# Kernel optimization log

Measured on AMD Instinct MI355X. Metric: run time of the kernel, lower is better.

The kernel has to match this reference:

```python
import jax, jax.numpy as jnp
import numpy as np

N_NODES, IN_F, HIDDEN, N_EDGES, N_TRAIN, N_CLASS = 50000, 64, 512, 160000, 80000, 7
BN_EPS = 1e-5

def _lin(k, fin, fout):
    return jax.random.normal(k, (fin, fout), jnp.float32) * 0.05, jnp.zeros((fout,), jnp.float32)

def setup_inputs() -> dict:
    key = jax.random.key(0)
    ks = jax.random.split(key, 12)
    x = jax.random.normal(ks[0], (N_NODES, IN_F), jnp.float32)
    edge_index = jax.random.randint(ks[1], (2, N_EDGES), 0, N_NODES, jnp.int32)
    train_edge_id = jax.random.randint(ks[2], (N_TRAIN,), 0, N_EDGES, jnp.int32)
    W1, b1 = _lin(ks[3], IN_F, HIDDEN)
    W2, b2 = _lin(ks[4], HIDDEN, HIDDEN)
    W3, b3 = _lin(ks[5], HIDDEN, HIDDEN)
    W4, b4 = _lin(ks[6], HIDDEN, HIDDEN)
    lin1_W, lin1_b = _lin(ks[7], HIDDEN, HIDDEN)
    lin2_W, lin2_b = _lin(ks[8], HIDDEN, HIDDEN)
    fc2_W, fc2_b = _lin(ks[9], HIDDEN, N_CLASS)
    ones = jnp.ones((HIDDEN,), jnp.float32); zeros = jnp.zeros((HIDDEN,), jnp.float32)
    return dict(x=x, edge_index=edge_index, train_edge_id=train_edge_id,
                W1=W1, b1=b1, W2=W2, b2=b2, W3=W3, b3=b3,
                bn1_g=ones, bn1_b=zeros, bn1_m=zeros, bn1_v=ones, eps1=jnp.float32(0.0),
                W4=W4, b4=b4, bn2_g=ones, bn2_b=zeros, bn2_m=zeros, bn2_v=ones, eps2=jnp.float32(0.0),
                lin1_W=lin1_W, lin1_b=lin1_b, lin2_W=lin2_W, lin2_b=lin2_b,
                fc2_W=fc2_W, fc2_b=fc2_b)

def _gin_agg(h, src, dst, eps):
    # PyG GINConv: (1+eps)*x_i + sum_{j in N(i)} x_j, messages flow src->dst
    agg = jax.ops.segment_sum(h[src], dst, num_segments=N_NODES)
    return (1.0 + eps) * h + agg

def _bn(h, g, b, m, v):
    return (h - m) * jax.lax.rsqrt(v + BN_EPS) * g + b

def reference(x, edge_index, train_edge_id, W1, b1, W2, b2, W3, b3,
              bn1_g, bn1_b, bn1_m, bn1_v, eps1,
              W4, b4, bn2_g, bn2_b, bn2_m, bn2_v, eps2,
              lin1_W, lin1_b, lin2_W, lin2_b, fc2_W, fc2_b):
    src, dst = edge_index[0], edge_index[1]
    h = _gin_agg(x, src, dst, eps1)
    h = jax.nn.relu(h @ W1 + b1)
    h = jax.nn.relu(h @ W2 + b2)
    h = jax.nn.relu(h @ W3 + b3)
    h = _bn(h, bn1_g, bn1_b, bn1_m, bn1_v)
    # gin_convs[0]: agg -> Linear+ReLU -> BN
    h = _gin_agg(h, src, dst, eps2)
    h = jax.nn.relu(h @ W4 + b4)
    h = _bn(h, bn2_g, bn2_b, bn2_m, bn2_v)
    # node MLP head (dropout = identity in eval)
    h = jax.nn.relu(h @ lin1_W + lin1_b)
    h = h @ lin2_W + lin2_b
    # edge-gather fusion (feature_fusion=None -> elementwise mul)
    node_id = edge_index[:, train_edge_id]  # [2, T]
    x1 = h[node_id[0]]
    x2 = h[node_id[1]]
    return (x1 * x2) @ fc2_W + fc2_b  # [T, class_num]
```

## Files before the change

kernel.cpp:

```cpp
#include <hip/hip_runtime.h>

#define N_NODES 50000
#define MPAD    50048
#define IN_F    64
#define HIDDEN  512
#define N_EDGES 160000
#define N_TRAIN 80000
#define N_CLASS 7
#define BN_EPS  1e-5f

#define MT      (MPAD / 128)
#define NT      4
#define FULLGRP ((MT / 8) * 32)

typedef short  bf16x8 __attribute__((ext_vector_type(8)));
typedef float  f32x4  __attribute__((ext_vector_type(4)));
typedef unsigned short ushort_t;

__device__ __forceinline__ ushort_t f2b(float v) {
    union { float f; unsigned int u; } c; c.f = v;
    unsigned int x = c.u;
    unsigned int r = (x + 0x7FFFu + ((x >> 16) & 1u)) >> 16;
    return (ushort_t)r;
}
__device__ __forceinline__ float b2f(ushort_t b) {
    union { unsigned int u; float f; } c; c.u = ((unsigned int)b) << 16;
    return c.f;
}

__device__ __forceinline__ void async_copy16(const void* g, void* l) {
    __builtin_amdgcn_global_load_lds(
        (const __attribute__((address_space(1))) void*)g,
        (__attribute__((address_space(3))) void*)l, 16, 0, 0);
}

__global__ void zero_kernel(int* __restrict__ p, int n) {
    int i = blockIdx.x * blockDim.x + threadIdx.x;
    if (i < n) p[i] = 0;
}

__global__ void hist_kernel(const int* __restrict__ ei, int* __restrict__ deg) {
    int e = blockIdx.x * blockDim.x + threadIdx.x;
    if (e >= N_EDGES) return;
    atomicAdd(&deg[ei[N_EDGES + e]], 1);
}

__global__ __launch_bounds__(1024) void scan_kernel(const int* __restrict__ deg,
                                                    int* __restrict__ rowptr) {
    __shared__ int buf[1024];
    __shared__ int carry_s;
    int tid = threadIdx.x;
    if (tid == 0) { carry_s = 0; rowptr[0] = 0; }
    __syncthreads();
    for (int base = 0; base < N_NODES; base += 1024) {
        int i = base + tid;
        buf[tid] = (i < N_NODES) ? deg[i] : 0;
        __syncthreads();
        for (int off = 1; off < 1024; off <<= 1) {
            int t = (tid >= off) ? buf[tid - off] : 0;
            __syncthreads();
            buf[tid] += t;
            __syncthreads();
        }
        if (i < N_NODES) rowptr[i + 1] = buf[tid] + carry_s;
        __syncthreads();
        if (tid == 0) carry_s += buf[1023];
        __syncthreads();
    }
}

__global__ void cursor_init_kernel(const int* __restrict__ rowptr,
                                   int* __restrict__ cursor) {
    int i = blockIdx.x * blockDim.x + threadIdx.x;
    if (i < N_NODES) cursor[i] = rowptr[i];
}

__global__ void scatter_kernel(const int* __restrict__ ei,
                               int* __restrict__ cursor, int* __restrict__ adj) {
    int e = blockIdx.x * blockDim.x + threadIdx.x;
    if (e >= N_EDGES) return;
    int src = ei[e], dst = ei[N_EDGES + e];
    int pos = atomicAdd(&cursor[dst], 1);
    adj[pos] = src;
}

__global__ __launch_bounds__(256) void gather64_kernel(
    const float* __restrict__ x, const int* __restrict__ rowptr,
    const int* __restrict__ adj, const float* __restrict__ epsp,
    ushort_t* __restrict__ hi, ushort_t* __restrict__ lo) {
    int wave = threadIdx.x >> 6, lane = threadIdx.x & 63;
    int n = blockIdx.x * 4 + wave;
    if (n >= N_NODES) return;
    float s = 1.0f + *epsp;
    float sum = s * x[(size_t)n * IN_F + lane];
    int beg = rowptr[n], end = rowptr[n + 1];
    for (int k = beg; k < end; k++) {
        sum += x[(size_t)adj[k] * IN_F + lane];
    }
    ushort_t hb = f2b(sum);
    ushort_t lb = f2b(sum - b2f(hb));
    hi[(size_t)n * IN_F + lane] = hb;
    lo[(size_t)n * IN_F + lane] = lb;
}

__global__ __launch_bounds__(256) void gather512_kernel(
    const float* __restrict__ h, const int* __restrict__ rowptr,
    const int* __restrict__ adj, const float* __restrict__ epsp,
    ushort_t* __restrict__ hi, ushort_t* __restrict__ lo) {
    int wave = threadIdx.x >> 6, lane = threadIdx.x & 63;
    int n = blockIdx.x * 2 + (wave >> 1);
    if (n >= N_NODES) return;
    float s = 1.0f + *epsp;
    const int f = (wave & 1) * 256 + lane * 4;
    float4 a = *(const float4*)&h[(size_t)n * HIDDEN + f];
    float sum[4] = {s * a.x, s * a.y, s * a.z, s * a.w};
    int beg = rowptr[n], end = rowptr[n + 1];
    for (int k = beg; k < end; k++) {
        float4 b = *(const float4*)&h[(size_t)adj[k] * HIDDEN + f];
        sum[0] += b.x; sum[1] += b.y; sum[2] += b.z; sum[3] += b.w;
    }
    ushort_t h4[4], l4[4];
#pragma unroll
    for (int j = 0; j < 4; j++) {
        h4[j] = f2b(sum[j]);
        l4[j] = f2b(sum[j] - b2f(h4[j]));
    }
    *(ushort4*)&hi[(size_t)n * HIDDEN + f] = make_ushort4(h4[0], h4[1], h4[2], h4[3]);
    *(ushort4*)&lo[(size_t)n * HIDDEN + f] = make_ushort4(l4[0], l4[1], l4[2], l4[3]);
}

__global__ void wtrans_kernel(const float* __restrict__ W,
                              ushort_t* __restrict__ Whi,
                              ushort_t* __restrict__ Wlo, int K) {
    __shared__ float t[32][33];
    int tx = threadIdx.x & 31, ty = threadIdx.x >> 5;
    int nb = blockIdx.x * 32, kb = blockIdx.y * 32;
#pragma unroll
    for (int i = 0; i < 4; i++) {
        int k = kb + ty + i * 8;
        t[ty + i * 8][tx] = W[(size_t)k * HIDDEN + nb + tx];
    }
    __syncthreads();
#pragma unroll
    for (int i = 0; i < 4; i++) {
        int n = nb + ty + i * 8;
        int k = kb + tx;
        float v = t[tx][ty + i * 8];
        ushort_t hb = f2b(v);
        ushort_t lb = f2b(v - b2f(hb));
        Whi[(size_t)n * K + k] = hb;
        Wlo[(size_t)n * K + k] = lb;
    }
}

template<int K>
__global__ __launch_bounds__(256) void gemm_split_kernel(
    const ushort_t* __restrict__ Ahi, const ushort_t* __restrict__ Alo,
    const ushort_t* __restrict__ Bhi, const ushort_t* __restrict__ Blo,
    const float* __restrict__ bias,
    float* __restrict__ Cf, ushort_t* __restrict__ Chi, ushort_t* __restrict__ Clo,
    int mode,
    const float* __restrict__ bn_g, const float* __restrict__ bn_b,
    const float* __restrict__ bn_m, const float* __restrict__ bn_v) {
    __shared__ ushort_t As_h[128 * 32];
    __shared__ ushort_t As_l[128 * 32];
    __shared__ ushort_t Bs_h[128 * 32];
    __shared__ ushort_t Bs_l[128 * 32];

    const int tid  = threadIdx.x;
    const int wave = tid >> 6, lane = tid & 63;
    const int wm = wave >> 1, wn = wave & 1;
    const int quad = lane >> 4, r = lane & 15;

    int idx = blockIdx.x, m_t, n_t;
    if (idx < FULLGRP) {
        m_t = (idx >> 5) * 8 + (idx & 7);
        n_t = (idx >> 3) & 3;
    } else {
        int t = idx - FULLGRP;
        m_t = (FULLGRP >> 2) + (t >> 2);
        n_t = t & 3;
    }
    const int m0 = m_t * 128, n0 = n_t * 128;

    const f32x4 vzero = {0.f, 0.f, 0.f, 0.f};
    f32x4 acc[4][4];
#pragma unroll
    for (int i = 0; i < 4; i++)
#pragma unroll
        for (int j = 0; j < 4; j++) acc[i][j] = vzero;

    const int srow = lane >> 2;
    const int scol = (((lane & 3) + ((srow >> 1) & 3)) & 3) * 8;
    const int csw  = ((quad - ((r >> 1) & 3)) & 3) * 8;

    for (int k0 = 0; k0 < K; k0 += 32) {
        __syncthreads();
#pragma unroll
        for (int tt = 0; tt < 2; tt++) {
            int rr = wave * 32 + tt * 16 + srow;
            int lbase = (wave * 32 + tt * 16) * 32;
            size_t ga = (size_t)(m0 + rr) * K + k0 + scol;
            size_t gb = (size_t)(n0 + rr) * K + k0 + scol;
            async_copy16(Ahi + ga, &As_h[lbase]);
            async_copy16(Alo + ga, &As_l[lbase]);
            async_copy16(Bhi + gb, &Bs_h[lbase]);
            async_copy16(Blo + gb, &Bs_l[lbase]);
        }
        __syncthreads();

        bf16x8 ah[4], al[4], bh[4], bl[4];
#pragma unroll
        for (int i = 0; i < 4; i++) {
            int aofs = (wm * 64 + i * 16 + r) * 32 + csw;
            int bofs = (wn * 64 + i * 16 + r) * 32 + csw;
            ah[i] = *(const bf16x8*)&As_h[aofs];
            al[i] = *(const bf16x8*)&As_l[aofs];
            bh[i] = *(const bf16x8*)&Bs_h[bofs];
            bl[i] = *(const bf16x8*)&Bs_l[bofs];
        }
#pragma unroll
        for (int i = 0; i < 4; i++)
#pragma unroll
            for (int j = 0; j < 4; j++) {
                acc[i][j] = __builtin_amdgcn_mfma_f32_16x16x32_bf16(ah[i], bh[j], acc[i][j], 0, 0, 0);
                acc[i][j] = __builtin_amdgcn_mfma_f32_16x16x32_bf16(ah[i], bl[j], acc[i][j], 0, 0, 0);
                acc[i][j] = __builtin_amdgcn_mfma_f32_16x16x32_bf16(al[i], bh[j], acc[i][j], 0, 0, 0);
            }
    }

    float bia[4], sc[4], sh[4];
#pragma unroll
    for (int j = 0; j < 4; j++) {
        int col = n0 + wn * 64 + j * 16 + r;
        bia[j] = bias[col];
        if (mode == 2) {
            float g = bn_g[col], bb = bn_b[col], mm = bn_m[col], vv = bn_v[col];
            sc[j] = g * rsqrtf(vv + BN_EPS);
            sh[j] = bb - mm * sc[j];
        } else { sc[j] = 1.f; sh[j] = 0.f; }
    }
#pragma unroll
    for (int i = 0; i < 4; i++) {
#pragma unroll
        for (int rg = 0; rg < 4; rg++) {
            int row = m0 + wm * 64 + i * 16 + quad * 4 + rg;
            if (row >= N_NODES) continue;
#pragma unroll
            for (int j = 0; j < 4; j++) {
                int col = n0 + wn * 64 + j * 16 + r;
                float v = acc[i][j][rg] + bia[j];
                if (mode >= 1) v = fmaxf(v, 0.f);
                if (mode == 2) v = v * sc[j] + sh[j];
                size_t oix = (size_t)row * HIDDEN + col;
                if (Cf) {
                    Cf[oix] = v;
                } else {
                    ushort_t hb = f2b(v);
                    ushort_t lb = f2b(v - b2f(hb));
                    Chi[oix] = hb;
                    Clo[oix] = lb;
                }
            }
        }
    }
}

__global__ __launch_bounds__(256) void fc2_kernel(
    const float* __restrict__ h, const int* __restrict__ ei,
    const int* __restrict__ teid, const float* __restrict__ W,
    const float* __restrict__ bias, float* __restrict__ out) {
    __shared__ float Ws[HIDDEN * N_CLASS];
    __shared__ float bs[N_CLASS];
    for (int i = threadIdx.x; i < HIDDEN * N_CLASS; i += blockDim.x) Ws[i] = W[i];
    if (threadIdx.x < N_CLASS) bs[threadIdx.x] = bias[threadIdx.x];
    __syncthreads();

    int wave = threadIdx.x >> 6;
    int lane = threadIdx.x & 63;
    int t = blockIdx.x * 4 + wave;
    if (t >= N_TRAIN) return;

    int e = teid[t];
    int a = ei[e];
    int b = ei[N_EDGES + e];
    const float* xa = h + (size_t)a * HIDDEN;
    const float* xb = h + (size_t)b * HIDDEN;

    float acc[N_CLASS];
#pragma unroll
    for (int c = 0; c < N_CLASS; c++) acc[c] = 0.f;

    int j0 = lane * 8;
    float4 a0 = *(const float4*)&xa[j0];
    float4 a1 = *(const float4*)&xa[j0 + 4];
    float4 b0 = *(const float4*)&xb[j0];
    float4 b1 = *(const float4*)&xb[j0 + 4];
    float p[8] = {a0.x * b0.x, a0.y * b0.y, a0.z * b0.z, a0.w * b0.w,
                  a1.x * b1.x, a1.y * b1.y, a1.z * b1.z, a1.w * b1.w};
#pragma unroll
    for (int jj = 0; jj < 8; jj++) {
        const float* wrow = &Ws[(j0 + jj) * N_CLASS];
#pragma unroll
        for (int c = 0; c < N_CLASS; c++) acc[c] = fmaf(p[jj], wrow[c], acc[c]);
    }
#pragma unroll
    for (int c = 0; c < N_CLASS; c++) {
        float v = acc[c];
        for (int off = 32; off > 0; off >>= 1) v += __shfl_down(v, off, 64);
        if (lane == 0) out[(size_t)t * N_CLASS + c] = v + bs[c];
    }
}

extern "C" void kernel_launch(void* const* d_in, const int* in_sizes, int n_in,
                              void* d_out, int out_size, void* d_ws, size_t ws_size,
                              hipStream_t stream) {
    const float* x      = (const float*)d_in[0];
    const int*   ei     = (const int*)d_in[1];
    const int*   teid   = (const int*)d_in[2];
    const float* W1     = (const float*)d_in[3];
    const float* b1     = (const float*)d_in[4];
    const float* W2     = (const float*)d_in[5];
    const float* b2     = (const float*)d_in[6];
    const float* W3     = (const float*)d_in[7];
    const float* b3     = (const float*)d_in[8];
    const float* bn1_g  = (const float*)d_in[9];
    const float* bn1_b  = (const float*)d_in[10];
    const float* bn1_m  = (const float*)d_in[11];
    const float* bn1_v  = (const float*)d_in[12];
    const float* eps1   = (const float*)d_in[13];
    const float* W4     = (const float*)d_in[14];
    const float* b4     = (const float*)d_in[15];
    const float* bn2_g  = (const float*)d_in[16];
    const float* bn2_b  = (const float*)d_in[17];
    const float* bn2_m  = (const float*)d_in[18];
    const float* bn2_v  = (const float*)d_in[19];
    const float* eps2   = (const float*)d_in[20];
    const float* lin1_W = (const float*)d_in[21];
    const float* lin1_b = (const float*)d_in[22];
    const float* lin2_W = (const float*)d_in[23];
    const float* lin2_b = (const float*)d_in[24];
    const float* fc2_W  = (const float*)d_in[25];
    const float* fc2_b  = (const float*)d_in[26];

    const size_t PLANE   = (size_t)MPAD * HIDDEN;
    const size_t PLANE64 = (size_t)MPAD * IN_F;

    ushort_t* R0h = (ushort_t*)d_ws;
    ushort_t* R0l = R0h + PLANE;
    ushort_t* R1h = R0l + PLANE;
    ushort_t* R1l = R1h + PLANE;

    const size_t WSMALL = (size_t)HIDDEN * IN_F;
    const size_t WBIG   = (size_t)HIDDEN * HIDDEN;
    ushort_t* Wp   = R1l + PLANE;
    ushort_t* Wt1h = Wp;            ushort_t* Wt1l = Wt1h + WSMALL;
    ushort_t* Wt2h = Wt1l + WSMALL; ushort_t* Wt2l = Wt2h + WBIG;
    ushort_t* Wt3h = Wt2l + WBIG;   ushort_t* Wt3l = Wt3h + WBIG;
    ushort_t* Wt4h = Wt3l + WBIG;   ushort_t* Wt4l = Wt4h + WBIG;
    ushort_t* Wt5h = Wt4l + WBIG;   ushort_t* Wt5l = Wt5h + WBIG;
    ushort_t* Wt6h = Wt5l + WBIG;   ushort_t* Wt6l = Wt6h + WBIG;

    int* deg    = (int*)(Wt6l + WBIG);
    int* rowptr = deg + N_NODES;
    int* adj    = rowptr + (N_NODES + 1);

    float* F32_R0 = (float*)R0h;
    ushort_t* H0h = R1h;
    ushort_t* H0l = R1h + PLANE64;

    zero_kernel<<<(N_NODES + 255) / 256, 256, 0, stream>>>(deg, N_NODES);
    hist_kernel<<<(N_EDGES + 255) / 256, 256, 0, stream>>>(ei, deg);
    scan_kernel<<<1, 1024, 0, stream>>>(deg, rowptr);
    cursor_init_kernel<<<(N_NODES + 255) / 256, 256, 0, stream>>>(rowptr, deg);
    scatter_kernel<<<(N_EDGES + 255) / 256, 256, 0, stream>>>(ei, deg, adj);

    dim3 wtgS(HIDDEN / 32, IN_F / 32);
    dim3 wtgB(HIDDEN / 32, HIDDEN / 32);
    wtrans_kernel<<<wtgS, 256, 0, stream>>>(W1, Wt1h, Wt1l, IN_F);
    wtrans_kernel<<<wtgB, 256, 0, stream>>>(W2, Wt2h, Wt2l, HIDDEN);
    wtrans_kernel<<<wtgB, 256, 0, stream>>>(W3, Wt3h, Wt3l, HIDDEN);
    wtrans_kernel<<<wtgB, 256, 0, stream>>>(W4, Wt4h, Wt4l, HIDDEN);
    wtrans_kernel<<<wtgB, 256, 0, stream>>>(lin1_W, Wt5h, Wt5l, HIDDEN);
    wtrans_kernel<<<wtgB, 256, 0, stream>>>(lin2_W, Wt6h, Wt6l, HIDDEN);

    const int ngrid = MT * NT;
    int nwb = (N_NODES + 3) / 4;

    gather64_kernel<<<nwb, 256, 0, stream>>>(x, rowptr, adj, eps1, H0h, H0l);

    gemm_split_kernel<IN_F><<<ngrid, 256, 0, stream>>>(H0h, H0l, Wt1h, Wt1l, b1,
        nullptr, R0h, R0l, 1, nullptr, nullptr, nullptr, nullptr);
    gemm_split_kernel<HIDDEN><<<ngrid, 256, 0, stream>>>(R0h, R0l, Wt2h, Wt2l, b2,
        nullptr, R1h, R1l, 1, nullptr, nullptr, nullptr, nullptr);
    gemm_split_kernel<HIDDEN><<<ngrid, 256, 0, stream>>>(R1h, R1l, Wt3h, Wt3l, b3,
        F32_R0, nullptr, nullptr, 2, bn1_g, bn1_b, bn1_m, bn1_v);

    gather512_kernel<<<(N_NODES + 1) / 2, 256, 0, stream>>>(F32_R0, rowptr, adj,
                                                            eps2, R1h, R1l);

    gemm_split_kernel<HIDDEN><<<ngrid, 256, 0, stream>>>(R1h, R1l, Wt4h, Wt4l, b4,
        nullptr, R0h, R0l, 2, bn2_g, bn2_b, bn2_m, bn2_v);
    gemm_split_kernel<HIDDEN><<<ngrid, 256, 0, stream>>>(R0h, R0l, Wt5h, Wt5l, lin1_b,
        nullptr, R1h, R1l, 1, nullptr, nullptr, nullptr, nullptr);
    gemm_split_kernel<HIDDEN><<<ngrid, 256, 0, stream>>>(R1h, R1l, Wt6h, Wt6l, lin2_b,
        F32_R0, nullptr, nullptr, 0, nullptr, nullptr, nullptr, nullptr);

    fc2_kernel<<<(N_TRAIN + 3) / 4, 256, 0, stream>>>(F32_R0, ei, teid, fc2_W, fc2_b,
                                                      (float*)d_out);
}
```

Measured before the change: 1.036 ms.

## Parallelize CSR scan, batch weight transposes, add specialized K=64 GEMM

Replaces the single-block serial prefix scan over 50k degrees with a three-kernel block-sum / scan / rowptr scheme that also writes the scatter cursors, which removes the cursor init kernel. The six weight-transpose launches are merged into one 3D-grid launch. The first layer's K=64 GEMM gets a dedicated kernel that loads the whole K slab into LDS in a single pass, with no pipelining loop. Together these cut launch count and serial preprocessing latency, at the cost of more code paths.

Result: faster. 933.0 us (median of 2 runs) (-10.0%).

```diff
diff --git a/kernel.cpp b/kernel.cpp
--- a/kernel.cpp
+++ b/kernel.cpp
@@ -12,6 +12,7 @@
 #define MT      (MPAD / 128)
 #define NT      4
 #define FULLGRP ((MT / 8) * 32)
+#define NBLK    ((N_NODES + 255) / 256)
 
 typedef short  bf16x8 __attribute__((ext_vector_type(8)));
 typedef float  f32x4  __attribute__((ext_vector_type(4)));
@@ -45,34 +46,56 @@
     atomicAdd(&deg[ei[N_EDGES + e]], 1);
 }
 
-__global__ __launch_bounds__(1024) void scan_kernel(const int* __restrict__ deg,
-                                                    int* __restrict__ rowptr) {
-    __shared__ int buf[1024];
-    __shared__ int carry_s;
+__global__ __launch_bounds__(256) void blocksum_kernel(const int* __restrict__ deg,
+                                                       int* __restrict__ bsum) {
+    __shared__ int s[256];
+    int i = blockIdx.x * 256 + threadIdx.x;
+    s[threadIdx.x] = (i < N_NODES) ? deg[i] : 0;
+    __syncthreads();
+    for (int off = 128; off > 0; off >>= 1) {
+        if (threadIdx.x < off) s[threadIdx.x] += s[threadIdx.x + off];
+        __syncthreads();
+    }
+    if (threadIdx.x == 0) bsum[blockIdx.x] = s[0];
+}
+
+__global__ __launch_bounds__(256) void scanbsum_kernel(const int* __restrict__ bsum,
+                                                       int* __restrict__ boff) {
+    __shared__ int s[256];
     int tid = threadIdx.x;
-    if (tid == 0) { carry_s = 0; rowptr[0] = 0; }
+    s[tid] = (tid < NBLK) ? bsum[tid] : 0;
     __syncthreads();
-    for (int base = 0; base < N_NODES; base += 1024) {
-        int i = base + tid;
-        buf[tid] = (i < N_NODES) ? deg[i] : 0;
-        __syncthreads();
-        for (int off = 1; off < 1024; off <<= 1) {
-            int t = (tid >= off) ? buf[tid - off] : 0;
-            __syncthreads();
-            buf[tid] += t;
-            __syncthreads();
-        }
-        if (i < N_NODES) rowptr[i + 1] = buf[tid] + carry_s;
-        __syncthreads();
-        if (tid == 0) carry_s += buf[1023];
-        __syncthreads();
-    }
-}
-
-__global__ void cursor_init_kernel(const int* __restrict__ rowptr,
-                                   int* __restrict__ cursor) {
-    int i = blockIdx.x * blockDim.x + threadIdx.x;
-    if (i < N_NODES) cursor[i] = rowptr[i];
+    for (int off = 1; off < 256; off <<= 1) {
+        int t = (tid >= off) ? s[tid - off] : 0;
+        __syncthreads();
+        s[tid] += t;
+        __syncthreads();
+    }
+    if (tid < NBLK) boff[tid] = (tid == 0) ? 0 : s[tid - 1];
+}
+
+__global__ __launch_bounds__(256) void rowptr_kernel(const int* __restrict__ deg,
+                                                     const int* __restrict__ boff,
+                                                     int* __restrict__ rowptr,
+                                                     int* __restrict__ cursor) {
+    __shared__ int s[256];
+    int tid = threadIdx.x;
+    int i = blockIdx.x * 256 + tid;
+    int d = (i < N_NODES) ? deg[i] : 0;
+    s[tid] = d;
+    __syncthreads();
+    for (int off = 1; off < 256; off <<= 1) {
+        int t = (tid >= off) ? s[tid - off] : 0;
+        __syncthreads();
+        s[tid] += t;
+        __syncthreads();
+    }
+    int incl = s[tid] + boff[blockIdx.x];
+    if (i < N_NODES) {
+        rowptr[i + 1] = incl;
+        cursor[i] = incl - d;
+    }
+    if (i == 0) rowptr[0] = 0;
 }
 
 __global__ void scatter_kernel(const int* __restrict__ ei,
@@ -129,12 +152,27 @@
     *(ushort4*)&lo[(size_t)n * HIDDEN + f] = make_ushort4(l4[0], l4[1], l4[2], l4[3]);
 }
 
-__global__ void wtrans_kernel(const float* __restrict__ W,
-                              ushort_t* __restrict__ Whi,
-                              ushort_t* __restrict__ Wlo, int K) {
+__global__ void wtrans_all_kernel(const float* __restrict__ w0,
+                                  const float* __restrict__ w1,
+                                  const float* __restrict__ w2,
+                                  const float* __restrict__ w3,
+                                  const float* __restrict__ w4,
+                                  const float* __restrict__ w5,
+                                  ushort_t* __restrict__ Wp) {
+    const size_t WSMALL = (size_t)HIDDEN * IN_F;
+    const size_t WBIG   = (size_t)HIDDEN * HIDDEN;
+    int z = blockIdx.z;
+    const float* W = (z == 0) ? w0 : (z == 1) ? w1 : (z == 2) ? w2
+                   : (z == 3) ? w3 : (z == 4) ? w4 : w5;
+    int K = (z == 0) ? IN_F : HIDDEN;
+    size_t off_h = (z == 0) ? 0 : 2 * WSMALL + (size_t)(z - 1) * 2 * WBIG;
+    ushort_t* Whi = Wp + off_h;
+    ushort_t* Wlo = Whi + ((z == 0) ? WSMALL : WBIG);
+
     __shared__ float t[32][33];
     int tx = threadIdx.x & 31, ty = threadIdx.x >> 5;
     int nb = blockIdx.x * 32, kb = blockIdx.y * 32;
+    if (kb >= K) return;
 #pragma unroll
     for (int i = 0; i < 4; i++) {
         int k = kb + ty + i * 8;
@@ -261,6 +299,103 @@
                     Chi[oix] = hb;
                     Clo[oix] = lb;
                 }
+            }
+        }
+    }
+}
+
+__global__ __launch_bounds__(256) void gemm_k64_kernel(
+    const ushort_t* __restrict__ Ahi, const ushort_t* __restrict__ Alo,
+    const ushort_t* __restrict__ Bhi, const ushort_t* __restrict__ Blo,
+    const float* __restrict__ bias,
+    ushort_t* __restrict__ Chi, ushort_t* __restrict__ Clo) {
+    const int K = 64;
+    __shared__ ushort_t As_h[128 * 64];
+    __shared__ ushort_t As_l[128 * 64];
+    __shared__ ushort_t Bs_h[128 * 64];
+    __shared__ ushort_t Bs_l[128 * 64];
+
+    const int tid  = threadIdx.x;
+    const int wave = tid >> 6, lane = tid & 63;
+    const int wm = wave >> 1, wn = wave & 1;
+    const int quad = lane >> 4, r = lane & 15;
+
+    int idx = blockIdx.x, m_t, n_t;
+    if (idx < FULLGRP) {
+        m_t = (idx >> 5) * 8 + (idx & 7);
+        n_t = (idx >> 3) & 3;
+    } else {
+        int t = idx - FULLGRP;
+        m_t = (FULLGRP >> 2) + (t >> 2);
+        n_t = t & 3;
+    }
+    const int m0 = m_t * 128, n0 = n_t * 128;
+
+    const int srow8 = lane >> 3;
+    const int sc8   = (((lane & 7) - srow8) & 7) * 8;
+#pragma unroll
+    for (int t = 0; t < 4; t++) {
+        int base = wave * 32 + t * 8;
+        int rr = base + srow8;
+        int lbase = base * 64;
+        size_t ga = (size_t)(m0 + rr) * K + sc8;
+        size_t gb = (size_t)(n0 + rr) * K + sc8;
+        async_copy16(Ahi + ga, &As_h[lbase]);
+        async_copy16(Alo + ga, &As_l[lbase]);
+        async_copy16(Bhi + gb, &Bs_h[lbase]);
+        async_copy16(Blo + gb, &Bs_l[lbase]);
+    }
+    __syncthreads();
+
+    const f32x4 vzero = {0.f, 0.f, 0.f, 0.f};
+    f32x4 acc[4][4];
+#pragma unroll
+    for (int i = 0; i < 4; i++)
+#pragma unroll
+        for (int j = 0; j < 4; j++) acc[i][j] = vzero;
+
+#pragma unroll
+    for (int ks = 0; ks < 2; ks++) {
+        bf16x8 ah[4], al[4], bh[4], bl[4];
+#pragma unroll
+        for (int i = 0; i < 4; i++) {
+            int ra = wm * 64 + i * 16 + r;
+            int rb = wn * 64 + i * 16 + r;
+            int ca = ((quad + ks * 4 + (ra & 7)) & 7) * 8;
+            int cb = ((quad + ks * 4 + (rb & 7)) & 7) * 8;
+            ah[i] = *(const bf16x8*)&As_h[ra * 64 + ca];
+            al[i] = *(const bf16x8*)&As_l[ra * 64 + ca];
+            bh[i] = *(const bf16x8*)&Bs_h[rb * 64 + cb];
+            bl[i] = *(const bf16x8*)&Bs_l[rb * 64 + cb];
+        }
+#pragma unroll
+        for (int i = 0; i < 4; i++)
+#pragma unroll
+            for (int j = 0; j < 4; j++) {
+                acc[i][j] = __builtin_amdgcn_mfma_f32_16x16x32_bf16(ah[i], bh[j], acc[i][j], 0, 0, 0);
+                acc[i][j] = __builtin_amdgcn_mfma_f32_16x16x32_bf16(ah[i], bl[j], acc[i][j], 0, 0, 0);
+                acc[i][j] = __builtin_amdgcn_mfma_f32_16x16x32_bf16(al[i], bh[j], acc[i][j], 0, 0, 0);
+            }
+    }
+
+    float bia[4];
+#pragma unroll
+    for (int j = 0; j < 4; j++) bia[j] = bias[n0 + wn * 64 + j * 16 + r];
+#pragma unroll
+    for (int i = 0; i < 4; i++) {
+#pragma unroll
+        for (int rg = 0; rg < 4; rg++) {
+            int row = m0 + wm * 64 + i * 16 + quad * 4 + rg;
+            if (row >= N_NODES) continue;
+#pragma unroll
+            for (int j = 0; j < 4; j++) {
+                int col = n0 + wn * 64 + j * 16 + r;
+                float v = fmaxf(acc[i][j][rg] + bia[j], 0.f);
+                size_t oix = (size_t)row * HIDDEN + col;
+                ushort_t hb = f2b(v);
+                ushort_t lb = f2b(v - b2f(hb));
+                Chi[oix] = hb;
+                Clo[oix] = lb;
             }
         }
     }
@@ -362,8 +497,11 @@
     ushort_t* Wt6h = Wt5l + WBIG;   ushort_t* Wt6l = Wt6h + WBIG;
 
     int* deg    = (int*)(Wt6l + WBIG);
-    int* rowptr = deg + N_NODES;
-    int* adj    = rowptr + (N_NODES + 1);
+    int* cursor = deg + N_NODES;
+    int* rowptr = cursor + N_NODES;
+    int* bsum   = rowptr + (N_NODES + 1);
+    int* boff   = bsum + NBLK;
+    int* adj    = boff + NBLK;
 
     float* F32_R0 = (float*)R0h;
     ushort_t* H0h = R1h;
@@ -371,26 +509,20 @@
 
     zero_kernel<<<(N_NODES + 255) / 256, 256, 0, stream>>>(deg, N_NODES);
     hist_kernel<<<(N_EDGES + 255) / 256, 256, 0, stream>>>(ei, deg);
-    scan_kernel<<<1, 1024, 0, stream>>>(deg, rowptr);
-    cursor_init_kernel<<<(N_NODES + 255) / 256, 256, 0, stream>>>(rowptr, deg);
-    scatter_kernel<<<(N_EDGES + 255) / 256, 256, 0, stream>>>(ei, deg, adj);
-
-    dim3 wtgS(HIDDEN / 32, IN_F / 32);
-    dim3 wtgB(HIDDEN / 32, HIDDEN / 32);
-    wtrans_kernel<<<wtgS, 256, 0, stream>>>(W1, Wt1h, Wt1l, IN_F);
-    wtrans_kernel<<<wtgB, 256, 0, stream>>>(W2, Wt2h, Wt2l, HIDDEN);
-    wtrans_kernel<<<wtgB, 256, 0, stream>>>(W3, Wt3h, Wt3l, HIDDEN);
-    wtrans_kernel<<<wtgB, 256, 0, stream>>>(W4, Wt4h, Wt4l, HIDDEN);
-    wtrans_kernel<<<wtgB, 256, 0, stream>>>(lin1_W, Wt5h, Wt5l, HIDDEN);
-    wtrans_kernel<<<wtgB, 256, 0, stream>>>(lin2_W, Wt6h, Wt6l, HIDDEN);
+    blocksum_kernel<<<NBLK, 256, 0, stream>>>(deg, bsum);
+    scanbsum_kernel<<<1, 256, 0, stream>>>(bsum, boff);
+    rowptr_kernel<<<NBLK, 256, 0, stream>>>(deg, boff, rowptr, cursor);
+    scatter_kernel<<<(N_EDGES + 255) / 256, 256, 0, stream>>>(ei, cursor, adj);
+
+    wtrans_all_kernel<<<dim3(16, 16, 6), 256, 0, stream>>>(W1, W2, W3, W4,
+                                                           lin1_W, lin2_W, Wp);
 
     const int ngrid = MT * NT;
     int nwb = (N_NODES + 3) / 4;
 
     gather64_kernel<<<nwb, 256, 0, stream>>>(x, rowptr, adj, eps1, H0h, H0l);
 
-    gemm_split_kernel<IN_F><<<ngrid, 256, 0, stream>>>(H0h, H0l, Wt1h, Wt1l, b1,
-        nullptr, R0h, R0l, 1, nullptr, nullptr, nullptr, nullptr);
+    gemm_k64_kernel<<<ngrid, 256, 0, stream>>>(H0h, H0l, Wt1h, Wt1l, b1, R0h, R0l);
     gemm_split_kernel<HIDDEN><<<ngrid, 256, 0, stream>>>(R0h, R0l, Wt2h, Wt2l, b2,
         nullptr, R1h, R1l, 1, nullptr, nullptr, nullptr, nullptr);
     gemm_split_kernel<HIDDEN><<<ngrid, 256, 0, stream>>>(R1h, R1l, Wt3h, Wt3l, b3,
```
